# Kernel optimization log

Measured on AMD Instinct MI355X. Metric: run time of the kernel, lower is better.

## Reference

```python
import jax, jax.numpy as jnp
import numpy as np

N_NODES = 20000
N_EDGES = 320000
F = 128            # dim == output_dim
L = 3              # num_layers
N_AGG, N_SCALER = 5, 3
POST_IN = F * (N_AGG * N_SCALER + 1)   # cat([x, scaled_agg])

# deg histogram passed to PNAConv -> avg log-degree constant (PyG: mean of log(bin+1))
_DEG_HIST = np.ones(33, dtype=np.float64)
AVG_LOG = float((np.log(np.arange(33) + 1.0) * _DEG_HIST).sum() / _DEG_HIST.sum())


def _init_linear(k, shape):
    # shape (..., fan_in, fan_out); Kaiming-uniform-ish scale on fan_in
    bound = 1.0 / np.sqrt(shape[-2])
    return jax.random.uniform(k, shape, jnp.float32, -bound, bound)


def setup_inputs() -> dict:
    key = jax.random.key(0)
    ks = jax.random.split(key, 10)
    return {
        "x": jax.random.normal(ks[0], (N_NODES, F), jnp.float32),
        "edge_index": jax.random.randint(ks[1], (2, N_EDGES), 0, N_NODES, jnp.int64),
        "W_pre": _init_linear(ks[2], (L, 2 * F, F)),      # pre_nn Linear(2F->F) per layer
        "b_pre": jnp.zeros((L, F), jnp.float32),
        "W_post": _init_linear(ks[3], (L, POST_IN, F)),   # post_nn Linear(16F->F)
        "b_post": jnp.zeros((L, F), jnp.float32),
        "W_lin": _init_linear(ks[4], (L, F, F)),          # PNAConv.lin Linear(F->F)
        "b_lin": jnp.zeros((L, F), jnp.float32),
        "W_out": _init_linear(ks[5], (F, 1)),             # output_layer
        "b_out": jnp.zeros((1,), jnp.float32),
    }


def reference(x, edge_index, W_pre, b_pre, W_post, b_post, W_lin, b_lin, W_out, b_out):
    n = x.shape[0]
    src, dst = edge_index[0], edge_index[1]  # x_j = x[src], x_i = x[dst]; aggregate onto dst

    # degree-based scalers (graph-fixed)
    cnt = jax.ops.segment_sum(jnp.ones((src.shape[0],), x.dtype), dst, num_segments=n)
    deg = jnp.clip(cnt, 1.0)[:, None]           # PyG clamps deg to >= 1
    log_deg = jnp.log(deg + 1.0)
    amp = log_deg / AVG_LOG                     # amplification scaler
    att = AVG_LOG / log_deg                     # attenuation scaler
    iso = (cnt == 0)[:, None]                   # isolated nodes -> min/max aggregates are 0

    for l in range(W_pre.shape[0]):
        # message: pre_nn(cat([x_i, x_j]))  -> [E, F]
        h = jnp.concatenate([x[dst], x[src]], axis=-1) @ W_pre[l] + b_pre[l]

        s = jax.ops.segment_sum(h, dst, num_segments=n)
        mean = s / deg
        mean_sq = jax.ops.segment_sum(h * h, dst, num_segments=n) / deg
        std = jnp.sqrt(jax.nn.relu(mean_sq - mean * mean) + 1e-5)
        mn = jnp.where(iso, 0.0, jax.ops.segment_min(h, dst, num_segments=n))
        mx = jnp.where(iso, 0.0, jax.ops.segment_max(h, dst, num_segments=n))

        agg = jnp.concatenate([mean, s, std, mn, mx], axis=-1)          # [N, 5F]
        scaled = jnp.concatenate([agg, agg * amp, agg * att], axis=-1)  # [N, 15F]

        out = jnp.concatenate([x, scaled], axis=-1) @ W_post[l] + b_post[l]
        x = jax.nn.relu(out @ W_lin[l] + b_lin[l])

    return jnp.squeeze(x @ W_out + b_out)  # target_dim == 1 -> [N]
```

## Files before the change

### kernel.cpp

```cpp
#include <hip/hip_runtime.h>
#include <math.h>

#define NN 20000
#define NE 320000
#define F 128
#define NLAYER 3
#define MPAD 20032
#define MROWS 20096
#define SCAN_NB 79

typedef unsigned int u32;
typedef unsigned short u16;
typedef __attribute__((ext_vector_type(8))) short bf16x8;
typedef __attribute__((ext_vector_type(4))) float f32x4;

__device__ __forceinline__ u16 f2bf(float f) {
    union { float f; u32 u; } x{f};
    u32 r = x.u + 0x7FFFu + ((x.u >> 16) & 1u);
    return (u16)(r >> 16);
}
__device__ __forceinline__ float bflo(u32 u) { return __uint_as_float(u << 16); }
__device__ __forceinline__ float bfhi(u32 u) { return __uint_as_float(u & 0xFFFF0000u); }

__device__ __forceinline__ void gload16(const u16* g, u16* l) {
    __builtin_amdgcn_global_load_lds(
        (const __attribute__((address_space(1))) void*)g,
        (__attribute__((address_space(3))) void*)l, 16, 0, 0);
}


__global__ void hist_kernel(const int* __restrict__ dst, int* __restrict__ cnt, int e) {
    int i = blockIdx.x * blockDim.x + threadIdx.x;
    if (i < e) atomicAdd(&cnt[dst[i]], 1);
}

__global__ void scan_p1(const int* __restrict__ cnt, int* __restrict__ bsum) {
    __shared__ int sh[256];
    int i = blockIdx.x * 256 + threadIdx.x;
    int t = threadIdx.x;
    sh[t] = (i < NN) ? cnt[i] : 0;
    __syncthreads();
#pragma unroll
    for (int d = 128; d > 0; d >>= 1) {
        if (t < d) sh[t] += sh[t + d];
        __syncthreads();
    }
    if (t == 0) bsum[blockIdx.x] = sh[0];
}

__global__ void scan_p23(const int* __restrict__ cnt, const int* __restrict__ bsum,
                         int* __restrict__ off, float* __restrict__ amp,
                         float* __restrict__ att, float avg_log) {
    __shared__ int sh[256];
    __shared__ int sb[128];
    int i = blockIdx.x * 256 + threadIdx.x;
    int t = threadIdx.x;
    if (t < 128) sb[t] = (t < SCAN_NB) ? bsum[t] : 0;
    __syncthreads();
#pragma unroll
    for (int d = 1; d < 128; d <<= 1) {
        int x = (t >= d && t < 128) ? sb[t - d] : 0;
        __syncthreads();
        if (t < 128) sb[t] += x;
        __syncthreads();
    }
    int base = (blockIdx.x == 0) ? 0 : sb[blockIdx.x - 1];
    int v = (i < NN) ? cnt[i] : 0;
    sh[t] = v;
    __syncthreads();
#pragma unroll
    for (int d = 1; d < 256; d <<= 1) {
        int x = (t >= d) ? sh[t - d] : 0;
        __syncthreads();
        sh[t] += x;
        __syncthreads();
    }
    if (i < NN) {
        int incl = sh[t] + base;
        off[i] = incl - v;
        if (i == NN - 1) off[NN] = incl;
        float deg = fmaxf((float)v, 1.0f);
        float ld = logf(deg + 1.0f);
        amp[i] = ld / avg_log;
        att[i] = avg_log / ld;
    }
}

__global__ void scatter_kernel(const int* __restrict__ src, const int* __restrict__ dst,
                               const int* __restrict__ off, int* __restrict__ cur,
                               int* __restrict__ csr, int e) {
    int i = blockIdx.x * blockDim.x + threadIdx.x;
    if (i < e) {
        int d = dst[i];
        int p = atomicAdd(&cur[d], 1);
        csr[off[d] + p] = src[i];
    }
}


#define P0 2560000L
#define P1 (P0 + 3L * 256 * 128)
#define P2 (P1 + 3L * 128 * 128)
#define P3 (P2 + 3L * 2048 * 128)
#define P4 (P3 + 3L * 256)
#define P5 (P4 + 3L * 128)
#define P6 (P5 + 2L * NN)
#define P7 (P6 + NN)

__global__ void prep_all(const float* __restrict__ x, const float* __restrict__ W_pre,
                         const float* __restrict__ W_lin, const float* __restrict__ W_post,
                         const float* __restrict__ b_pre, const float* __restrict__ b_post,
                         const float* __restrict__ b_lin,
                         u16* __restrict__ xbuf,
                         u16* __restrict__ WpreT, u16* __restrict__ WlinT,
                         u16* __restrict__ Wpostb, float* __restrict__ biaspre,
                         float* __restrict__ bcomb,
                         int* __restrict__ cnt, int* __restrict__ cur,
                         float* __restrict__ y) {
    long i = (long)blockIdx.x * 256 + threadIdx.x;
    if (i < P0) {
        xbuf[i] = f2bf(x[i]);
    } else if (i < P1) {
        long j = i - P0;
        int l = j / 32768, t = j % 32768;
        int c = t >> 7, k = t & 127;
        int si = (c < 128) ? (k * 128 + c) : ((k + 128) * 128 + (c - 128));
        WpreT[l * 32768 + t] = f2bf(W_pre[l * 32768 + si]);
    } else if (i < P2) {
        long j = i - P1;
        int l = j / 16384, t = j % 16384;
        int c = t >> 7, k = t & 127;
        WlinT[l * 16384 + t] = f2bf(W_lin[l * 16384 + k * 128 + c]);
    } else if (i < P3) {
        long j = i - P2;
        Wpostb[j] = f2bf(W_post[j]);
    } else if (i < P4) {
        long j = i - P3;
        int l = j / 256, t = j % 256;
        biaspre[l * 256 + t] = (t < 128) ? b_pre[l * 128 + t] : 0.f;
    } else if (i < P5) {
        long j = i - P4;
        int l = j / 128, t = j % 128;
        float s = b_lin[l * 128 + t];
        for (int c = 0; c < 128; ++c) s += b_post[l * 128 + c] * W_lin[l * 16384 + c * 128 + t];
        bcomb[l * 128 + t] = s;
    } else if (i < P6) {
        long j = i - P5;
        if (j < NN) cnt[j] = 0; else cur[j - NN] = 0;
    } else if (i < P7) {
        y[i - P6] = 0.f;
    }
}


#define PROC(u) { float v_; \
    v_ = bflo(u); s0 += v_; q0 = fmaf(v_, v_, q0); mn0 = fminf(mn0, v_); mx0 = fmaxf(mx0, v_); \
    v_ = bfhi(u); s1 += v_; q1 = fmaf(v_, v_, q1); mn1 = fminf(mn1, v_); mx1 = fmaxf(mx1, v_); }

__global__ __launch_bounds__(256) void agg_kernel(
    const u16* __restrict__ preC, const u16* __restrict__ preB,
    const int* __restrict__ off, const int* __restrict__ csr,
    u16* __restrict__ aggb) {
    int tid = threadIdx.x, w = tid >> 6, lane = tid & 63;
    const u32* bpl = (const u32*)preB + lane;
    int nwaves = gridDim.x * 4;
    for (int node = blockIdx.x * 4 + w; node < NN; node += nwaves) {
        int o0 = off[node], o1 = off[node + 1];
        int deg = o1 - o0;
        float s0 = 0, s1 = 0, q0 = 0, q1 = 0;
        float mn0 = 1e30f, mn1 = 1e30f, mx0 = -1e30f, mx1 = -1e30f;
        int j = o0;
        int nb = deg >> 3;
        if (nb > 0) {
            int idx[8];
#pragma unroll
            for (int p = 0; p < 8; ++p) idx[p] = csr[j + p];
            for (int b = 1; b < nb; ++b) {
                u32 u[8];
#pragma unroll
                for (int p = 0; p < 8; ++p) u[p] = bpl[(size_t)idx[p] * 64];
#pragma unroll
                for (int p = 0; p < 8; ++p) idx[p] = csr[j + 8 * b + p];
#pragma unroll
                for (int p = 0; p < 8; ++p) PROC(u[p]);
            }
            {
                u32 u[8];
#pragma unroll
                for (int p = 0; p < 8; ++p) u[p] = bpl[(size_t)idx[p] * 64];
#pragma unroll
                for (int p = 0; p < 8; ++p) PROC(u[p]);
            }
            j += nb * 8;
        }
        if (j + 4 <= o1) {
            int i0 = csr[j], i1 = csr[j + 1], i2 = csr[j + 2], i3 = csr[j + 3];
            u32 u0 = bpl[(size_t)i0 * 64];
            u32 u1 = bpl[(size_t)i1 * 64];
            u32 u2 = bpl[(size_t)i2 * 64];
            u32 u3 = bpl[(size_t)i3 * 64];
            PROC(u0); PROC(u1); PROC(u2); PROC(u3);
            j += 4;
        }
        for (; j < o1; ++j) { u32 u = bpl[(size_t)csr[j] * 64]; PROC(u); }

        float mean0, mean1, sum0, sum1, std0, std1, lo0, lo1, hi0, hi1;
        if (deg == 0) {
            sum0 = sum1 = 0.f; mean0 = mean1 = 0.f;
            std0 = std1 = sqrtf(1e-5f);
            lo0 = lo1 = hi0 = hi1 = 0.f;
        } else {
            u32 uc = ((const u32*)preC)[(size_t)node * 64 + lane];
            float c0 = bflo(uc), c1 = bfhi(uc), dg = (float)deg;
            sum0 = dg * c0 + s0; mean0 = sum0 / dg;
            sum1 = dg * c1 + s1; mean1 = sum1 / dg;
            float msq0 = c0 * c0 + (2.f * c0 * s0 + q0) / dg;
            float msq1 = c1 * c1 + (2.f * c1 * s1 + q1) / dg;
            std0 = sqrtf(fmaxf(msq0 - mean0 * mean0, 0.f) + 1e-5f);
            std1 = sqrtf(fmaxf(msq1 - mean1 * mean1, 0.f) + 1e-5f);
            lo0 = c0 + mn0; lo1 = c1 + mn1; hi0 = c0 + mx0; hi1 = c1 + mx1;
        }
        u32* cr = (u32*)aggb + (size_t)node * 320 + lane;
        float f0[5] = {mean0, sum0, std0, lo0, hi0};
        float f1[5] = {mean1, sum1, std1, lo1, hi1};
#pragma unroll
        for (int a = 0; a < 5; ++a)
            cr[a * 64] = (u32)f2bf(f0[a]) | ((u32)f2bf(f1[a]) << 16);
    }
}


template <bool BIAS, int MODE, bool SWZ>
__global__ __launch_bounds__(256) void mfma_gemm(
    const u16* __restrict__ A, int lda,
    const u16* __restrict__ Bt, int K,
    const float* __restrict__ bias,
    u16* __restrict__ C, u16* __restrict__ C2, int ldc, int Mreal,
    size_t aS, size_t bS, size_t cS) {
    __shared__ u16 As[64 * 32];
    __shared__ u16 Bs[128 * 32];
    int row0, col0;
    if (SWZ) {
        int g = blockIdx.x;
        int row = (g >> 4) * 8 + (g & 7);
        if (row >= 313) return;
        row0 = row * 64;
        col0 = ((g >> 3) & 1) * 128;
    } else {
        row0 = blockIdx.x * 64;
        col0 = blockIdx.y * 128;
    }
    int z = blockIdx.z;
    A += (size_t)z * aS; Bt += (size_t)z * bS; C += (size_t)z * cS;
    int tid = threadIdx.x;
    int w = tid >> 6, lane = tid & 63;

    int arow = tid >> 2, asl = tid & 3;
    const u16* agp = A + (size_t)(row0 + arow) * lda + ((asl ^ ((arow >> 1) & 3)) << 3);
    u16* alds = As + w * 512;
    int br0 = tid >> 2;
    int br1 = 64 + (tid >> 2);
    const u16* bgp0 = Bt + (size_t)(col0 + br0) * K + (((tid & 3) ^ ((br0 >> 1) & 3)) << 3);
    const u16* bgp1 = Bt + (size_t)(col0 + br1) * K + (((tid & 3) ^ ((br1 >> 1) & 3)) << 3);
    u16* blds0 = Bs + w * 512;
    u16* blds1 = Bs + 2048 + w * 512;

    f32x4 acc[2][4];
#pragma unroll
    for (int m = 0; m < 2; ++m)
#pragma unroll
        for (int n = 0; n < 4; ++n) acc[m][n] = (f32x4){0.f, 0.f, 0.f, 0.f};

    int s = lane >> 4, r = lane & 15;
    int wr = (w >> 1) * 32, wc = (w & 1) * 64;

    for (int k0 = 0; k0 < K; k0 += 32) {
        gload16(agp + k0, alds);
        gload16(bgp0 + k0, blds0);
        gload16(bgp1 + k0, blds1);
        __syncthreads();
        bf16x8 a[2], b[4];
#pragma unroll
        for (int m = 0; m < 2; ++m) {
            int row = wr + m * 16 + r;
            a[m] = *(const bf16x8*)&As[row * 32 + ((s ^ ((row >> 1) & 3)) << 3)];
        }
#pragma unroll
        for (int n = 0; n < 4; ++n) {
            int col = wc + n * 16 + r;
            b[n] = *(const bf16x8*)&Bs[col * 32 + ((s ^ ((col >> 1) & 3)) << 3)];
        }
#pragma unroll
        for (int m = 0; m < 2; ++m)
#pragma unroll
            for (int n = 0; n < 4; ++n)
                acc[m][n] = __builtin_amdgcn_mfma_f32_16x16x32_bf16(a[m], b[n], acc[m][n], 0, 0, 0);
        __syncthreads();
    }

#pragma unroll
    for (int m = 0; m < 2; ++m) {
#pragma unroll
        for (int n = 0; n < 4; ++n) {
            int gcol = col0 + wc + n * 16 + r;
            float bs = BIAS ? bias[gcol] : 0.f;
#pragma unroll
            for (int j = 0; j < 4; ++j) {
                int grow = row0 + wr + m * 16 + s * 4 + j;
                if (grow < Mreal) {
                    u16 h = f2bf(acc[m][n][j] + bs);
                    if (MODE == 0) {
                        C[(size_t)grow * ldc + gcol] = h;
                    } else if (MODE == 2) {
                        if (gcol < 128) C[(size_t)grow * 128 + gcol] = h;
                        else            C2[(size_t)grow * 128 + gcol - 128] = h;
                    } else {
                        size_t idx;
                        if (gcol < 128) idx = (size_t)grow * 768 + gcol;
                        else {
                            int t2 = gcol - 128;
                            int gg = t2 / 640;
                            int ko = 128 + t2 - gg * 640;
                            idx = (size_t)(gg * 128 + grow) * 768 + ko;
                        }
                        C[idx] = h;
                    }
                }
            }
        }
    }
}


template <bool OUT>
__global__ __launch_bounds__(256) void comb2(
    const u16* __restrict__ xin,
    const u16* __restrict__ aggb,
    const u16* __restrict__ BtK,
    const float* __restrict__ bias,
    const float* __restrict__ amp, const float* __restrict__ att,
    u16* __restrict__ xout,
    const float* __restrict__ Wout,
    const float* __restrict__ bout,
    float* __restrict__ y) {
    __shared__ u16 S[3][10240];
    int g = blockIdx.x;
    int row = (g >> 4) * 8 + (g & 7);
    if (row >= 157) return;
    int row0 = row * 128;
    int cb = (g >> 3) & 1;
    int tid = threadIdx.x;
    int w = tid >> 6, lane = tid & 63;
    int r = lane & 15, s4 = lane >> 4;
    int wr = (w >> 1) * 64, wc = (w & 1) * 32;

    int rtA0 = tid >> 2, qA = tid & 3;
    int rtA1 = rtA0 + 64;
    int koffA0 = (qA ^ ((rtA0 >> 1) & 3)) << 3;
    int koffA1 = (qA ^ ((rtA1 >> 1) & 3)) << 3;
    const u16* xA0 = xin + (size_t)(row0 + rtA0) * 128 + koffA0;
    const u16* xA1 = xin + (size_t)(row0 + rtA1) * 128 + koffA1;
    const u16* gA0 = aggb + (size_t)(row0 + rtA0) * 640 + koffA0 - 128;
    const u16* gA1 = aggb + (size_t)(row0 + rtA1) * 640 + koffA1 - 128;
    const u16* bB[3];
#pragma unroll
    for (int p = 2; p < 5; ++p) {
        int lid = tid + 256 * p;
        int rt = lid >> 2, q = lid & 3;
        int rb = rt - 128, gg = rb >> 6, jj = rb & 63;
        int koff = (q ^ ((rt >> 1) & 3)) << 3;
        bB[p - 2] = BtK + (size_t)(gg * 128 + cb * 64 + jj) * 768 + koff;
    }

    f32x4 acc[4][3][2];
#pragma unroll
    for (int m = 0; m < 4; ++m)
#pragma unroll
        for (int gg = 0; gg < 3; ++gg)
#pragma unroll
            for (int n = 0; n < 2; ++n) acc[m][gg][n] = (f32x4){0.f, 0.f, 0.f, 0.f};

    auto STAGE = [&](int t, int b) {
        const u16* a0 = (t < 4) ? (xA0 + t * 32) : (gA0 + t * 32);
        const u16* a1 = (t < 4) ? (xA1 + t * 32) : (gA1 + t * 32);
        gload16(a0, &S[b][(size_t)tid * 8]);
        gload16(a1, &S[b][(size_t)(tid + 256) * 8]);
#pragma unroll
        for (int p = 2; p < 5; ++p)
            gload16(bB[p - 2] + t * 32, &S[b][(size_t)(tid + 256 * p) * 8]);
    };

    STAGE(0, 0);
    STAGE(1, 1);
    asm volatile("s_waitcnt vmcnt(5)" ::: "memory");
    __builtin_amdgcn_s_barrier();
    asm volatile("" ::: "memory");

    int buf = 0;
    for (int t = 0; t < 24; ++t) {
        if (t + 2 < 24) STAGE(t + 2, (t + 2) % 3);
        const u16* Sb = S[buf];
        bf16x8 a[4];
#pragma unroll
        for (int m = 0; m < 4; ++m) {
            int rw = wr + m * 16 + r;
            a[m] = *(const bf16x8*)&Sb[rw * 32 + ((s4 ^ ((rw >> 1) & 3)) << 3)];
        }
#pragma unroll
        for (int gg = 0; gg < 3; ++gg) {
            if (gg > 0 && t < 4) continue;
#pragma unroll
            for (int n = 0; n < 2; ++n) {
                int rb = gg * 64 + wc + n * 16 + r;
                bf16x8 b = *(const bf16x8*)&Sb[4096 + rb * 32 + ((s4 ^ ((rb >> 1) & 3)) << 3)];
#pragma unroll
                for (int m = 0; m < 4; ++m)
                    acc[m][gg][n] = __builtin_amdgcn_mfma_f32_16x16x32_bf16(a[m], b, acc[m][gg][n], 0, 0, 0);
            }
        }
        if (t < 23) {
            if (t + 2 < 24) asm volatile("s_waitcnt vmcnt(5)" ::: "memory");
            else            asm volatile("s_waitcnt vmcnt(0)" ::: "memory");
            __builtin_amdgcn_s_barrier();
            asm volatile("" ::: "memory");
        }
        buf = (buf == 2) ? 0 : buf + 1;
    }

    int gcb = cb * 64 + wc;
#pragma unroll
    for (int m = 0; m < 4; ++m)
#pragma unroll
        for (int j = 0; j < 4; ++j) {
            int grow = row0 + wr + m * 16 + s4 * 4 + j;
            if (grow >= NN) continue;
            float av = amp[grow], tv = att[grow];
            if (OUT) {
                float ps = 0.f;
#pragma unroll
                for (int n = 0; n < 2; ++n) {
                    int gcol = gcb + n * 16 + r;
                    float v = acc[m][0][n][j] + av * acc[m][1][n][j] + tv * acc[m][2][n][j] + bias[gcol];
                    v = fmaxf(v, 0.f);
                    ps = fmaf(v, Wout[gcol], ps);
                }
                ps += __shfl_xor(ps, 1, 16);
                ps += __shfl_xor(ps, 2, 16);
                ps += __shfl_xor(ps, 4, 16);
                ps += __shfl_xor(ps, 8, 16);
                if (r == 0) {
                    if (cb == 0 && wc == 0) ps += bout[0];
                    atomicAdd(&y[grow], ps);
                }
            } else {
#pragma unroll
                for (int n = 0; n < 2; ++n) {
                    int gcol = gcb + n * 16 + r;
                    float v = acc[m][0][n][j] + av * acc[m][1][n][j] + tv * acc[m][2][n][j] + bias[gcol];
                    v = fmaxf(v, 0.f);
                    xout[(size_t)grow * F + gcol] = f2bf(v);
                }
            }
        }
}


extern "C" void kernel_launch(void* const* d_in, const int* in_sizes, int n_in,
                              void* d_out, int out_size, void* d_ws, size_t ws_size,
                              hipStream_t stream) {
    const float* x_in   = (const float*)d_in[0];
    const int*   ei     = (const int*)d_in[1];
    const float* W_pre  = (const float*)d_in[2];
    const float* b_pre  = (const float*)d_in[3];
    const float* W_post = (const float*)d_in[4];
    const float* b_post = (const float*)d_in[5];
    const float* W_lin  = (const float*)d_in[6];
    const float* b_lin  = (const float*)d_in[7];
    const float* W_out  = (const float*)d_in[8];
    const float* b_out  = (const float*)d_in[9];

    const int* src = ei;
    const int* dst = ei + NE;

    double sl = 0.0;
    for (int i = 0; i < 33; ++i) sl += log((double)(i + 1));
    float avg_log = (float)(sl / 33.0);

    char* ws = (char*)d_ws;
    size_t p = 0;
    auto alloc = [&](size_t bytes) { void* r = ws + p; p += (bytes + 255) & ~(size_t)255; return r; };
    u16*   xbufA   = (u16*)alloc((size_t)MROWS * F * 2);
    u16*   xbufB   = (u16*)alloc((size_t)MROWS * F * 2);
    u16*   aggb    = (u16*)alloc((size_t)MROWS * 640 * 2);
    u16*   preC    = (u16*)alloc((size_t)MPAD * F * 2);
    u16*   preB    = (u16*)alloc((size_t)MPAD * F * 2);
    u16*   WpreT   = (u16*)alloc((size_t)3 * 256 * 128 * 2);
    u16*   Wpostb  = (u16*)alloc((size_t)3 * 2048 * 128 * 2);
    u16*   WlinT   = (u16*)alloc((size_t)3 * 128 * 128 * 2);
    u16*   BtK     = (u16*)alloc((size_t)3 * 384 * 768 * 2);
    float* biaspre = (float*)alloc((size_t)3 * 256 * 4);
    float* bcomb   = (float*)alloc((size_t)3 * 128 * 4);
    float* amp     = (float*)alloc((size_t)MPAD * 4);
    float* att     = (float*)alloc((size_t)MPAD * 4);
    int*   cnt     = (int*)alloc((size_t)NN * 4);
    int*   offs    = (int*)alloc((size_t)(NN + 1) * 4);
    int*   cur     = (int*)alloc((size_t)NN * 4);
    int*   csr     = (int*)alloc((size_t)NE * 4);
    int*   bsum    = (int*)alloc((size_t)SCAN_NB * 4);
    (void)ws_size;

    float* y = (float*)d_out;

    prep_all<<<(int)((P7 + 255) / 256), 256, 0, stream>>>(
        x_in, W_pre, W_lin, W_post, b_pre, b_post, b_lin,
        xbufA, WpreT, WlinT, Wpostb, biaspre, bcomb, cnt, cur, y);

    hist_kernel<<<(NE + 255) / 256, 256, 0, stream>>>(dst, cnt, NE);
    scan_p1<<<SCAN_NB, 256, 0, stream>>>(cnt, bsum);
    scan_p23<<<SCAN_NB, 256, 0, stream>>>(cnt, bsum, offs, amp, att, avg_log);
    scatter_kernel<<<(NE + 255) / 256, 256, 0, stream>>>(src, dst, offs, cur, csr, NE);

    mfma_gemm<false, 1, false><<<dim3(2, 16, 3), 256, 0, stream>>>(
        WlinT, 128, Wpostb, 128, nullptr, BtK, nullptr, 0, 128,
        16384, 262144, 294912);

    mfma_gemm<true, 2, true><<<640, 256, 0, stream>>>(
        xbufA, F, WpreT, 128, biaspre, preC, preB, 128, MPAD, 0, 0, 0);

    u16* xc = xbufA;
    u16* xn = xbufB;
    for (int l = 0; l < NLAYER; ++l) {
        agg_kernel<<<2048, 256, 0, stream>>>(preC, preB, offs, csr, aggb);
        if (l < NLAYER - 1) {
            comb2<false><<<320, 256, 0, stream>>>(
                xc, aggb, BtK + (size_t)l * 294912, bcomb + (size_t)l * 128,
                amp, att, xn, nullptr, nullptr, nullptr);
            mfma_gemm<true, 2, true><<<640, 256, 0, stream>>>(
                xn, F, WpreT + (size_t)(l + 1) * 32768, 128,
                biaspre + (size_t)(l + 1) * 256, preC, preB, 128, MPAD, 0, 0, 0);
            u16* tmp = xc; xc = xn; xn = tmp;
        } else {
            comb2<true><<<320, 256, 0, stream>>>(
                xc, aggb, BtK + (size_t)l * 294912, bcomb + (size_t)l * 128,
                amp, att, nullptr, W_out, b_out, y);
        }
    }
}
```

Baseline: 216.4 us.

## Replace pre-message GEMM with 128-row tiled kernel using triple-buffered async LDS pipeline

Adds a dedicated pre2 kernel for the per-layer node projection (x @ W_pre halves). It uses 128x128 output tiles per block with a 4x4 MFMA accumulator per wave and a three-stage async global-to-LDS pipeline with explicit vmcnt waits, instead of the generic 64x128 synchronous-load GEMM. The generic GEMM is stripped down to only the one-time weight-combination mode. Larger tiles raise data reuse and halve the block count, at the cost of more registers per thread and lower occupancy. The preC/preB buffers are enlarged to MROWS so the unguarded stores stay in bounds.

```diff
diff --git a/kernel.cpp b/kernel.cpp
--- a/kernel.cpp
+++ b/kernel.cpp
@@ -230,26 +230,14 @@
 }
 
 
-template <bool BIAS, int MODE, bool SWZ>
 __global__ __launch_bounds__(256) void mfma_gemm(
     const u16* __restrict__ A, int lda,
     const u16* __restrict__ Bt, int K,
-    const float* __restrict__ bias,
-    u16* __restrict__ C, u16* __restrict__ C2, int ldc, int Mreal,
+    u16* __restrict__ C, int Mreal,
     size_t aS, size_t bS, size_t cS) {
     __shared__ u16 As[64 * 32];
     __shared__ u16 Bs[128 * 32];
-    int row0, col0;
-    if (SWZ) {
-        int g = blockIdx.x;
-        int row = (g >> 4) * 8 + (g & 7);
-        if (row >= 313) return;
-        row0 = row * 64;
-        col0 = ((g >> 3) & 1) * 128;
-    } else {
-        row0 = blockIdx.x * 64;
-        col0 = blockIdx.y * 128;
-    }
+    int row0 = blockIdx.x * 64, col0 = blockIdx.y * 128;
     int z = blockIdx.z;
     A += (size_t)z * aS; Bt += (size_t)z * bS; C += (size_t)z * cS;
     int tid = threadIdx.x;
@@ -303,32 +291,112 @@
 #pragma unroll
         for (int n = 0; n < 4; ++n) {
             int gcol = col0 + wc + n * 16 + r;
-            float bs = BIAS ? bias[gcol] : 0.f;
 #pragma unroll
             for (int j = 0; j < 4; ++j) {
                 int grow = row0 + wr + m * 16 + s * 4 + j;
                 if (grow < Mreal) {
-                    u16 h = f2bf(acc[m][n][j] + bs);
-                    if (MODE == 0) {
-                        C[(size_t)grow * ldc + gcol] = h;
-                    } else if (MODE == 2) {
-                        if (gcol < 128) C[(size_t)grow * 128 + gcol] = h;
-                        else            C2[(size_t)grow * 128 + gcol - 128] = h;
-                    } else {
-                        size_t idx;
-                        if (gcol < 128) idx = (size_t)grow * 768 + gcol;
-                        else {
-                            int t2 = gcol - 128;
-                            int gg = t2 / 640;
-                            int ko = 128 + t2 - gg * 640;
-                            idx = (size_t)(gg * 128 + grow) * 768 + ko;
-                        }
-                        C[idx] = h;
+                    u16 h = f2bf(acc[m][n][j]);
+                    size_t idx;
+                    if (gcol < 128) idx = (size_t)grow * 768 + gcol;
+                    else {
+                        int t2 = gcol - 128;
+                        int gg = t2 / 640;
+                        int ko = 128 + t2 - gg * 640;
+                        idx = (size_t)(gg * 128 + grow) * 768 + ko;
                     }
+                    C[idx] = h;
                 }
             }
         }
     }
+}
+
+
+__global__ __launch_bounds__(256) void pre2(
+    const u16* __restrict__ xin,
+    const u16* __restrict__ Wp,
+    const float* __restrict__ biasl,
+    u16* __restrict__ preC, u16* __restrict__ preB) {
+    __shared__ u16 S[3][8192];
+    int g = blockIdx.x;
+    int row = (g >> 4) * 8 + (g & 7);
+    if (row >= 157) return;
+    int row0 = row * 128;
+    int cb = (g >> 3) & 1;
+    int tid = threadIdx.x;
+    int w = tid >> 6, lane = tid & 63;
+    int r = lane & 15, s4 = lane >> 4;
+    int wr = (w >> 1) * 64, wcb = (w & 1) * 64;
+
+    const u16* gp[4];
+#pragma unroll
+    for (int p = 0; p < 4; ++p) {
+        int lid = tid + 256 * p;
+        int rt = lid >> 2, q = lid & 3;
+        int koff = (q ^ ((rt >> 1) & 3)) << 3;
+        if (rt < 128) gp[p] = xin + (size_t)(row0 + rt) * 128 + koff;
+        else          gp[p] = Wp + (size_t)(cb * 128 + (rt - 128)) * 128 + koff;
+    }
+
+    f32x4 acc[4][4];
+#pragma unroll
+    for (int m = 0; m < 4; ++m)
+#pragma unroll
+        for (int n = 0; n < 4; ++n) acc[m][n] = (f32x4){0.f, 0.f, 0.f, 0.f};
+
+    auto STAGE = [&](int t, int b) {
+#pragma unroll
+        for (int p = 0; p < 4; ++p)
+            gload16(gp[p] + t * 32, &S[b][(size_t)(tid + 256 * p) * 8]);
+    };
+
+    STAGE(0, 0);
+    STAGE(1, 1);
+    asm volatile("s_waitcnt vmcnt(4)" ::: "memory");
+    __builtin_amdgcn_s_barrier();
+    asm volatile("" ::: "memory");
+
+    for (int t = 0; t < 4; ++t) {
+        if (t + 2 < 4) STAGE(t + 2, (t + 2) % 3);
+        const u16* Sb = S[t % 3];
+        bf16x8 a[4], b[4];
+#pragma unroll
+        for (int m = 0; m < 4; ++m) {
+            int rw = wr + m * 16 + r;
+            a[m] = *(const bf16x8*)&Sb[rw * 32 + ((s4 ^ ((rw >> 1) & 3)) << 3)];
+        }
+#pragma unroll
+        for (int n = 0; n < 4; ++n) {
+            int cB = wcb + n * 16 + r;
+            b[n] = *(const bf16x8*)&Sb[4096 + cB * 32 + ((s4 ^ ((cB >> 1) & 3)) << 3)];
+        }
+#pragma unroll
+        for (int m = 0; m < 4; ++m)
+#pragma unroll
+            for (int n = 0; n < 4; ++n)
+                acc[m][n] = __builtin_amdgcn_mfma_f32_16x16x32_bf16(a[m], b[n], acc[m][n], 0, 0, 0);
+        if (t < 3) {
+            if (t + 2 < 4) asm volatile("s_waitcnt vmcnt(4)" ::: "memory");
+            else           asm volatile("s_waitcnt vmcnt(0)" ::: "memory");
+            __builtin_amdgcn_s_barrier();
+            asm volatile("" ::: "memory");
+        }
+    }
+
+    u16* out = cb ? preB : preC;
+    const float* bs = biasl + cb * 128;
+#pragma unroll
+    for (int m = 0; m < 4; ++m)
+#pragma unroll
+        for (int n = 0; n < 4; ++n) {
+            int gcol = wcb + n * 16 + r;
+            float bv = bs[gcol];
+#pragma unroll
+            for (int j = 0; j < 4; ++j) {
+                int grow = row0 + wr + m * 16 + s4 * 4 + j;
+                out[(size_t)grow * 128 + gcol] = f2bf(acc[m][n][j] + bv);
+            }
+        }
 }
 
 
@@ -492,8 +560,8 @@
     u16*   xbufA   = (u16*)alloc((size_t)MROWS * F * 2);
     u16*   xbufB   = (u16*)alloc((size_t)MROWS * F * 2);
     u16*   aggb    = (u16*)alloc((size_t)MROWS * 640 * 2);
-    u16*   preC    = (u16*)alloc((size_t)MPAD * F * 2);
-    u16*   preB    = (u16*)alloc((size_t)MPAD * F * 2);
+    u16*   preC    = (u16*)alloc((size_t)MROWS * F * 2);
+    u16*   preB    = (u16*)alloc((size_t)MROWS * F * 2);
     u16*   WpreT   = (u16*)alloc((size_t)3 * 256 * 128 * 2);
     u16*   Wpostb  = (u16*)alloc((size_t)3 * 2048 * 128 * 2);
     u16*   WlinT   = (u16*)alloc((size_t)3 * 128 * 128 * 2);
@@ -520,12 +588,11 @@
     scan_p23<<<SCAN_NB, 256, 0, stream>>>(cnt, bsum, offs, amp, att, avg_log);
     scatter_kernel<<<(NE + 255) / 256, 256, 0, stream>>>(src, dst, offs, cur, csr, NE);
 
-    mfma_gemm<false, 1, false><<<dim3(2, 16, 3), 256, 0, stream>>>(
-        WlinT, 128, Wpostb, 128, nullptr, BtK, nullptr, 0, 128,
+    mfma_gemm<<<dim3(2, 16, 3), 256, 0, stream>>>(
+        WlinT, 128, Wpostb, 128, BtK, 128,
         16384, 262144, 294912);
 
-    mfma_gemm<true, 2, true><<<640, 256, 0, stream>>>(
-        xbufA, F, WpreT, 128, biaspre, preC, preB, 128, MPAD, 0, 0, 0);
+    pre2<<<320, 256, 0, stream>>>(xbufA, WpreT, biaspre, preC, preB);
 
     u16* xc = xbufA;
     u16* xn = xbufB;
@@ -535,9 +602,9 @@
             comb2<false><<<320, 256, 0, stream>>>(
                 xc, aggb, BtK + (size_t)l * 294912, bcomb + (size_t)l * 128,
                 amp, att, xn, nullptr, nullptr, nullptr);
-            mfma_gemm<true, 2, true><<<640, 256, 0, stream>>>(
-                xn, F, WpreT + (size_t)(l + 1) * 32768, 128,
-                biaspre + (size_t)(l + 1) * 256, preC, preB, 128, MPAD, 0, 0, 0);
+            pre2<<<320, 256, 0, stream>>>(
+                xn, WpreT + (size_t)(l + 1) * 32768, biaspre + (size_t)(l + 1) * 256,
+                preC, preB);
             u16* tmp = xc; xc = xn; xn = tmp;
         } else {
             comb2<true><<<320, 256, 0, stream>>>(
```

Result: no change. 212.3 us (-1.9%).
